# Kernel optimization log

Measured on AMD Instinct MI355X. Metric: run time of the kernel, lower is better.

Reference implementation:

```python
import jax, jax.numpy as jnp
import numpy as np

B, S, HID = 2, 2048, 2048
H, KV, D = 16, 4, 128
ROT = 64           # partial rotary dim (= cos.shape[-1])
EMB = 128          # router embedding dim
TAU, BASE = 0.4, 3.0
EPS = 1e-6


def rotate_half(x):
    h = x.shape[-1] // 2
    return jnp.concatenate([-x[..., h:], x[..., :h]], axis=-1)


def rmsnorm(x, w, eps=EPS):
    # Qwen3.5: zero-init weight, (1 + w) scaling, compute in fp32
    xf = x.astype(jnp.float32)
    o = xf * jax.lax.rsqrt(jnp.mean(xf * xf, axis=-1, keepdims=True) + eps)
    return (o * (1.0 + w.astype(jnp.float32))).astype(x.dtype)


def _rope_tables():
    inv_freq = 1.0 / (10000.0 ** (np.arange(0, ROT, 2, dtype=np.float32) / ROT))
    t = np.arange(S, dtype=np.float32)
    freqs = np.outer(t, inv_freq)                 # [S, ROT/2]
    emb = np.concatenate([freqs, freqs], axis=-1)  # [S, ROT]
    cos = np.broadcast_to(np.cos(emb), (B, S, ROT)).copy()
    sin = np.broadcast_to(np.sin(emb), (B, S, ROT)).copy()
    return jnp.asarray(cos), jnp.asarray(sin)


def setup_inputs() -> dict:
    key = jax.random.key(0)
    ks = jax.random.split(key, 10)
    sc = 0.02
    cos, sin = _rope_tables()
    return {
        "hidden_states": jax.random.normal(ks[0], (B, S, HID), jnp.float32),
        "cos": cos,
        "sin": sin,
        # projection weights stored as [in, out] (torch Linear weight transposed)
        "Wq": jax.random.normal(ks[1], (HID, H * D * 2), jnp.float32) * sc,
        "Wk": jax.random.normal(ks[2], (HID, KV * D), jnp.float32) * sc,
        "Wv": jax.random.normal(ks[3], (HID, KV * D), jnp.float32) * sc,
        "Wo": jax.random.normal(ks[4], (H * D, HID), jnp.float32) * sc,
        "q_norm_w": jnp.zeros((D,), jnp.float32),
        "k_norm_w": jnp.zeros((D,), jnp.float32),
        "Wr": jax.random.normal(ks[5], (HID, EMB), jnp.float32) * sc,   # router linear
        "Wd": jax.random.normal(ks[6], (EMB, D), jnp.float32) * sc,     # router decoder
        "ln_g": jnp.ones((EMB,), jnp.float32),
        "ln_b": jnp.zeros((EMB,), jnp.float32),
        "rnn_state": jnp.zeros((EMB,), jnp.float32),
    }


def _forward(hidden_states, cos, sin, Wq, Wk, Wv, Wo, q_norm_w, k_norm_w,
             Wr, Wd, ln_g, ln_b, rnn_state):
    b, s, _ = hidden_states.shape
    # doubled q_proj -> query + gate
    qkv = jnp.einsum('bsh,hd->bsd', hidden_states, Wq).reshape(b, s, H, 2 * D)
    q, gate = qkv[..., :D], qkv[..., D:]
    gate = gate.reshape(b, s, H * D)
    k = jnp.einsum('bsh,hd->bsd', hidden_states, Wk).reshape(b, s, KV, D)
    v = jnp.einsum('bsh,hd->bsd', hidden_states, Wv).reshape(b, s, KV, D)
    # per-head RMSNorm then [b, h, s, d]
    q = rmsnorm(q, q_norm_w).transpose(0, 2, 1, 3)
    k = rmsnorm(k, k_norm_w).transpose(0, 2, 1, 3)
    v = v.transpose(0, 2, 1, 3)

    # --- head-dim router (gumbel-sigmoid, straight-through hard round) ---
    emb = jnp.einsum('bsh,he->bse', hidden_states, Wr) + rnn_state
    mu = jnp.mean(emb, -1, keepdims=True)
    var = jnp.mean((emb - mu) ** 2, -1, keepdims=True)
    ln = (emb - mu) * jax.lax.rsqrt(var + 1e-5) * ln_g + ln_b
    logits = jnp.einsum('bse,ed->bsd', jax.nn.gelu(ln, approximate=False), Wd)
    gum = -jnp.log(jax.random.exponential(jax.random.key(42), logits.shape, jnp.float32))
    y_soft = jax.nn.sigmoid((logits + gum + BASE) / TAU)
    binary = jax.lax.stop_gradient(jnp.round(y_soft) - y_soft) + y_soft  # [b, s, D]
    mask = binary[:, None, :, :]  # broadcast over heads: [b, 1, s, D]

    q = q * mask
    k = k * mask

    # partial RoPE on first ROT dims (qk_index=None training path)
    c = cos[:, None, :, :]
    si = sin[:, None, :, :]
    def rope(x):
        xr, xp = x[..., :ROT], x[..., ROT:]
        return jnp.concatenate([xr * c + rotate_half(xr) * si, xp], axis=-1)
    q = rope(q)
    k = rope(k)

    # GQA: repeat kv heads
    rep = H // KV
    k = jnp.repeat(k, rep, axis=1)
    v = jnp.repeat(v, rep, axis=1)

    scores = jnp.einsum('bhqd,bhkd->bhqk', q, k) / np.sqrt(D).astype(np.float32)
    causal = jnp.tril(jnp.ones((s, s), bool))
    scores = jnp.where(causal, scores, jnp.finfo(jnp.float32).min)
    attn = jax.nn.softmax(scores.astype(jnp.float32), axis=-1).astype(q.dtype)
    out = jnp.einsum('bhqk,bhkd->bhqd', attn, v)
    out = out.transpose(0, 2, 1, 3).reshape(b, s, H * D)
    out = out * jax.nn.sigmoid(gate)   # output gate
    return jnp.einsum('bsd,dh->bsh', out, Wo)


def reference(hidden_states, cos, sin, Wq, Wk, Wv, Wo, q_norm_w, k_norm_w,
              Wr, Wd, ln_g, ln_b, rnn_state):
    return _forward(hidden_states, cos, sin, Wq, Wk, Wv, Wo, q_norm_w, k_norm_w,
                    Wr, Wd, ln_g, ln_b, rnn_state)
```

## Files before the change

kernel.cpp:

```cpp
#include <hip/hip_runtime.h>
#include <math.h>

typedef __bf16 bf16;
typedef bf16 bf16x8 __attribute__((ext_vector_type(8)));
typedef bf16 bf16x4 __attribute__((ext_vector_type(4)));
typedef float f32x4 __attribute__((ext_vector_type(4)));

#define BB 2
#define SS 2048
#define HIDN 2048
#define NH 16
#define NKV 4
#define DD 128
#define NROT 64
#define NPROJ 5248

__device__ __forceinline__ float waveAllReduceSum(float v) {
#pragma unroll
  for (int o = 1; o < 64; o <<= 1) v += __shfl_xor(v, o, 64);
  return v;
}

__device__ __forceinline__ int xcd_swz(int orig, int nwg) {
  return (orig & 7) * (nwg >> 3) + (orig >> 3);
}

__device__ __forceinline__ void gload16(const bf16* g, bf16* l) {
  __builtin_amdgcn_global_load_lds((const __attribute__((address_space(1))) void*)g,
                                   (__attribute__((address_space(3))) void*)l, 16, 0, 0);
}

__global__ __launch_bounds__(256) void cvt_bf16_k(const float* __restrict__ in,
                                                  bf16* __restrict__ out, int n) {
  int i = (blockIdx.x * 256 + threadIdx.x) * 4;
  if (i + 3 < n) {
    float4 v = *reinterpret_cast<const float4*>(in + i);
    bf16x4 o = {(bf16)v.x, (bf16)v.y, (bf16)v.z, (bf16)v.w};
    *reinterpret_cast<bf16x4*>(out + i) = o;
  }
}

__global__ __launch_bounds__(256) void transpose_cvt(const float* __restrict__ W,
                                                     bf16* __restrict__ WT, int K, int N,
                                                     int rowOff) {
  __shared__ bf16 tile[64][72];
  int n0 = blockIdx.x * 64, k0 = blockIdx.y * 64;
  int tx = threadIdx.x & 63, ty = threadIdx.x >> 6;
#pragma unroll
  for (int i = 0; i < 16; i++) {
    int k = ty + i * 4;
    tile[k][tx] = (bf16)W[(size_t)(k0 + k) * N + n0 + tx];
  }
  __syncthreads();
#pragma unroll
  for (int i = 0; i < 16; i++) {
    int n = ty + i * 4;
    WT[(size_t)(rowOff + n0 + n) * K + k0 + tx] = tile[tx][n];
  }
}

template <typename CT>
__global__ __launch_bounds__(256) void gemm_bt(const bf16* __restrict__ A,
                                               const bf16* __restrict__ Bt,
                                               CT* __restrict__ C, int M, int N, int K) {
  __shared__ bf16 lA[128 * 64];
  __shared__ bf16 lB[128 * 64];
  const int nbx = N >> 7;
  int wg = xcd_swz(blockIdx.x, gridDim.x);
  int bx = wg % nbx, by = wg / nbx;
  const int t = threadIdx.x;
  const int l = t & 63, w = t >> 6;
  const int wr = w >> 1, wc = w & 1;
  const int lr = l & 15, lhi = l >> 4;

  f32x4 acc[4][4];
#pragma unroll
  for (int m = 0; m < 4; m++)
#pragma unroll
    for (int n = 0; n < 4; n++) acc[m][n] = f32x4{0.f, 0.f, 0.f, 0.f};

  const int rowA0 = by * 128, rowB0 = bx * 128;
  const int nkt = K >> 6;
  for (int kt = 0; kt < nkt; ++kt) {
    __syncthreads();
#pragma unroll
    for (int it = 0; it < 4; ++it) {
      int slot = it * 256 + t;
      int row = slot >> 3, sl = slot & 7;
      gload16(A + (size_t)(rowA0 + row) * K + kt * 64 + ((sl ^ (row & 7)) << 3), lA + slot * 8);
      gload16(Bt + (size_t)(rowB0 + row) * K + kt * 64 + ((sl ^ (row & 7)) << 3), lB + slot * 8);
    }
    __syncthreads();
#pragma unroll
    for (int kc = 0; kc < 2; ++kc) {
      bf16x8 af[4], bg[4];
#pragma unroll
      for (int m = 0; m < 4; m++) {
        int row = wr * 64 + m * 16 + lr;
        af[m] = *reinterpret_cast<const bf16x8*>((char*)lA + row * 128 + (((kc * 4 + lhi) ^ (row & 7)) << 4));
      }
#pragma unroll
      for (int n = 0; n < 4; n++) {
        int row = wc * 64 + n * 16 + lr;
        bg[n] = *reinterpret_cast<const bf16x8*>((char*)lB + row * 128 + (((kc * 4 + lhi) ^ (row & 7)) << 4));
      }
      __builtin_amdgcn_s_setprio(1);
#pragma unroll
      for (int m = 0; m < 4; m++)
#pragma unroll
        for (int n = 0; n < 4; n++)
          acc[m][n] = __builtin_amdgcn_mfma_f32_16x16x32_bf16(af[m], bg[n], acc[m][n], 0, 0, 0);
      __builtin_amdgcn_s_setprio(0);
    }
  }
#pragma unroll
  for (int m = 0; m < 4; m++)
#pragma unroll
    for (int n = 0; n < 4; n++)
#pragma unroll
      for (int r = 0; r < 4; r++) {
        int grow = rowA0 + wr * 64 + m * 16 + lhi * 4 + r;
        int gcol = rowB0 + wc * 64 + n * 16 + lr;
        C[(size_t)grow * N + gcol] = (CT)acc[m][n][r];
      }
}

__device__ __forceinline__ unsigned rotl32(unsigned x, int r) { return (x << r) | (x >> (32 - r)); }

__device__ __forceinline__ float gumbel42(unsigned i) {
  const unsigned half = (unsigned)(BB * SS * DD) / 2u;
  unsigned x0, x1;
  int word;
  if (i < half) { x0 = i; x1 = i + half; word = 0; }
  else          { x0 = i - half; x1 = i; word = 1; }
  const unsigned k0 = 0u, k1 = 42u;
  const unsigned k2 = k0 ^ k1 ^ 0x1BD11BDAu;
  x0 += k0; x1 += k1;
#define TF_R(r) { x0 += x1; x1 = rotl32(x1, r); x1 ^= x0; }
  TF_R(13) TF_R(15) TF_R(26) TF_R(6)
  x0 += k1; x1 += k2 + 1u;
  TF_R(17) TF_R(29) TF_R(16) TF_R(24)
  x0 += k2; x1 += k0 + 2u;
  TF_R(13) TF_R(15) TF_R(26) TF_R(6)
  x0 += k0; x1 += k1 + 3u;
  TF_R(17) TF_R(29) TF_R(16) TF_R(24)
  x0 += k1; x1 += k2 + 4u;
  TF_R(13) TF_R(15) TF_R(26) TF_R(6)
  x0 += k2; x1 += k0 + 5u;
#undef TF_R
  unsigned bits = word ? x1 : x0;
  float u = __uint_as_float((bits >> 9) | 0x3f800000u) - 1.0f;
  float ex = -log1pf(-u);
  return -logf(ex);
}

__global__ __launch_bounds__(128) void mask_kernel(const bf16* __restrict__ qkva,
                                                   const float* __restrict__ rnn,
                                                   const float* __restrict__ lng,
                                                   const float* __restrict__ lnb,
                                                   const float* __restrict__ Wd,
                                                   bf16* __restrict__ maskb) {
  int row = blockIdx.x;
  int t = threadIdx.x;
  int l = t & 63, w = t >> 6;
  __shared__ float redm[2], redv[2], gsh[128];
  float e = (float)qkva[(size_t)row * NPROJ + 5120 + t] + rnn[t];
  float s1 = waveAllReduceSum(e);
  if (l == 0) redm[w] = s1;
  __syncthreads();
  float mu = (redm[0] + redm[1]) * (1.0f / 128.0f);
  float dv = (e - mu) * (e - mu);
  float s2 = waveAllReduceSum(dv);
  if (l == 0) redv[w] = s2;
  __syncthreads();
  float var = (redv[0] + redv[1]) * (1.0f / 128.0f);
  float ln = (e - mu) * rsqrtf(var + 1e-5f) * lng[t] + lnb[t];
  float g = 0.5f * ln * (1.0f + erff(ln * 0.7071067811865475f));
  gsh[t] = g;
  __syncthreads();
  float logit = 0.f;
#pragma unroll 8
  for (int e2 = 0; e2 < 128; e2++) logit += gsh[e2] * Wd[e2 * 128 + t];
  float gum = gumbel42((unsigned)(row * 128 + t));
  float x = (logit + gum + 3.0f) * 2.5f;
  float y = 1.0f / (1.0f + expf(-x));
  maskb[(size_t)row * 128 + t] = (bf16)rintf(y);
}

__global__ __launch_bounds__(256) void qgate_kernel(const bf16* __restrict__ qkva,
                                                    const bf16* __restrict__ maskb,
                                                    const float* __restrict__ qw,
                                                    const float* __restrict__ cosT,
                                                    const float* __restrict__ sinT,
                                                    bf16* __restrict__ wq,
                                                    bf16* __restrict__ sgate) {
  int t = threadIdx.x;
  int g = t >> 4, ln = t & 15;
  int hr = blockIdx.x * 16 + g;
  int h = hr & 15, row = hr >> 4;
  int b = row >> 11, s = row & 2047;
  const bf16* qp = qkva + (size_t)row * NPROJ + h * 256 + ln * 8;
  bf16x8 q8 = *reinterpret_cast<const bf16x8*>(qp);
  bf16x8 g8 = *reinterpret_cast<const bf16x8*>(qp + 128);
  bf16x8 m8 = *reinterpret_cast<const bf16x8*>(maskb + (size_t)row * 128 + ln * 8);
  float qf[8], ss = 0.f;
#pragma unroll
  for (int j = 0; j < 8; j++) { qf[j] = (float)q8[j]; ss += qf[j] * qf[j]; }
#pragma unroll
  for (int o = 1; o < 16; o <<= 1) ss += __shfl_xor(ss, o, 16);
  float rinv = rsqrtf(ss * (1.0f / 128.0f) + 1e-6f);
  alignas(16) float wv[8];
  const float4* qw4 = reinterpret_cast<const float4*>(qw);
  *reinterpret_cast<float4*>(&wv[0]) = qw4[ln * 2];
  *reinterpret_cast<float4*>(&wv[4]) = qw4[ln * 2 + 1];
  float qm[8];
#pragma unroll
  for (int j = 0; j < 8; j++) qm[j] = qf[j] * rinv * (1.0f + wv[j]) * (float)m8[j];
  alignas(16) float c8[8], s8[8];
  if (ln < 8) {
    const float4* c4 = reinterpret_cast<const float4*>(cosT + (size_t)row * 64);
    const float4* sn4 = reinterpret_cast<const float4*>(sinT + (size_t)row * 64);
    *reinterpret_cast<float4*>(&c8[0]) = c4[ln * 2];
    *reinterpret_cast<float4*>(&c8[4]) = c4[ln * 2 + 1];
    *reinterpret_cast<float4*>(&s8[0]) = sn4[ln * 2];
    *reinterpret_cast<float4*>(&s8[4]) = sn4[ln * 2 + 1];
  }
  float po[8];
#pragma unroll
  for (int j = 0; j < 8; j++) po[j] = __shfl_xor(qm[j], 4, 16);
  bf16x8 oq, og;
#pragma unroll
  for (int j = 0; j < 8; j++) {
    float ov;
    if (ln < 4) ov = qm[j] * c8[j] - po[j] * s8[j];
    else if (ln < 8) ov = qm[j] * c8[j] + po[j] * s8[j];
    else ov = qm[j];
    oq[j] = (bf16)(ov * 0.08838834764831845f);
    og[j] = (bf16)(1.0f / (1.0f + expf(-(float)g8[j])));
  }
  size_t o = ((size_t)((b * 16 + h) * 2048 + s)) * 128 + ln * 8;
  *reinterpret_cast<bf16x8*>(wq + o) = oq;
  *reinterpret_cast<bf16x8*>(sgate + o) = og;
}

__global__ __launch_bounds__(256) void k_kernel(const bf16* __restrict__ qkva,
                                                const bf16* __restrict__ maskb,
                                                const float* __restrict__ kw,
                                                const float* __restrict__ cosT,
                                                const float* __restrict__ sinT,
                                                bf16* __restrict__ wk) {
  int t = threadIdx.x;
  int g = t >> 4, ln = t & 15;
  int hr = blockIdx.x * 16 + g;
  int kv = hr & 3, row = hr >> 2;
  int b = row >> 11, s = row & 2047;
  const bf16* kp = qkva + (size_t)row * NPROJ + 4096 + kv * 128 + ln * 8;
  bf16x8 k8 = *reinterpret_cast<const bf16x8*>(kp);
  bf16x8 m8 = *reinterpret_cast<const bf16x8*>(maskb + (size_t)row * 128 + ln * 8);
  float kf[8], ss = 0.f;
#pragma unroll
  for (int j = 0; j < 8; j++) { kf[j] = (float)k8[j]; ss += kf[j] * kf[j]; }
#pragma unroll
  for (int o = 1; o < 16; o <<= 1) ss += __shfl_xor(ss, o, 16);
  float rinv = rsqrtf(ss * (1.0f / 128.0f) + 1e-6f);
  alignas(16) float wv[8];
  const float4* kw4 = reinterpret_cast<const float4*>(kw);
  *reinterpret_cast<float4*>(&wv[0]) = kw4[ln * 2];
  *reinterpret_cast<float4*>(&wv[4]) = kw4[ln * 2 + 1];
  float km[8];
#pragma unroll
  for (int j = 0; j < 8; j++) km[j] = kf[j] * rinv * (1.0f + wv[j]) * (float)m8[j];
  alignas(16) float c8[8], s8[8];
  if (ln < 8) {
    const float4* c4 = reinterpret_cast<const float4*>(cosT + (size_t)row * 64);
    const float4* sn4 = reinterpret_cast<const float4*>(sinT + (size_t)row * 64);
    *reinterpret_cast<float4*>(&c8[0]) = c4[ln * 2];
    *reinterpret_cast<float4*>(&c8[4]) = c4[ln * 2 + 1];
    *reinterpret_cast<float4*>(&s8[0]) = sn4[ln * 2];
    *reinterpret_cast<float4*>(&s8[4]) = sn4[ln * 2 + 1];
  }
  float po[8];
#pragma unroll
  for (int j = 0; j < 8; j++) po[j] = __shfl_xor(km[j], 4, 16);
  bf16x8 ok;
#pragma unroll
  for (int j = 0; j < 8; j++) {
    float ov;
    if (ln < 4) ov = km[j] * c8[j] - po[j] * s8[j];
    else if (ln < 8) ov = km[j] * c8[j] + po[j] * s8[j];
    else ov = km[j];
    ok[j] = (bf16)ov;
  }
  *reinterpret_cast<bf16x8*>(wk + ((size_t)((b * 4 + kv) * 2048 + s)) * 128 + ln * 8) = ok;
}

__global__ __launch_bounds__(256) void vt_kernel(const bf16* __restrict__ qkva,
                                                 bf16* __restrict__ wvt) {
  int dt = blockIdx.x & 1;
  int st = (blockIdx.x >> 1) & 31;
  int bkv = blockIdx.x >> 6;
  int b = bkv >> 2, kv = bkv & 3;
  __shared__ bf16 tl[64][72];
  int tx = threadIdx.x & 63, ty = threadIdx.x >> 6;
  int s0 = st * 64, d0 = dt * 64;
#pragma unroll
  for (int i = 0; i < 16; i++) {
    int srow = ty + i * 4;
    tl[srow][tx] = qkva[(size_t)(b * 2048 + s0 + srow) * NPROJ + 4608 + kv * 128 + d0 + tx];
  }
  __syncthreads();
#pragma unroll
  for (int i = 0; i < 16; i++) {
    int drow = ty + i * 4;
    wvt[(size_t)((b * 4 + kv) * 128 + d0 + drow) * 2048 + s0 + tx] = tl[tx][drow];
  }
}

__global__ __launch_bounds__(256) void attn_kernel(const bf16* __restrict__ wq,
                                                   const bf16* __restrict__ wk,
                                                   const bf16* __restrict__ wvt,
                                                   const bf16* __restrict__ sgate,
                                                   bf16* __restrict__ wattn) {
  __shared__ bf16 lK[64 * 128];
  __shared__ bf16 lV[128 * 64];
  __shared__ bf16 lP[4][16 * 64];
  int wg = xcd_swz(blockIdx.x, 512);
  int pair = wg & 15;
  int bh = wg >> 4;
  int b = bh >> 4, h = bh & 15, kvh = h >> 2;
  int t = threadIdx.x, l = t & 63, w = t >> 6;
  int lr = l & 15, lhi = l >> 4;

  const bf16* kbase = wk + (size_t)((b * 4 + kvh) * 2048) * 128;
  const bf16* vbase = wvt + (size_t)((b * 4 + kvh) * 128) * 2048;
  char* pb = (char*)(&lP[w][0]);

  for (int half = 0; half < 2; ++half) {
    int qb = half ? (31 - pair) : pair;
    const bf16* qbase = wq + (size_t)((b * 16 + h) * 2048 + qb * 64 + w * 16) * 128;
    bf16x8 aq[4];
#pragma unroll
    for (int kc = 0; kc < 4; kc++)
      aq[kc] = *reinterpret_cast<const bf16x8*>(qbase + (size_t)lr * 128 + kc * 32 + lhi * 8);

    f32x4 oacc[8];
#pragma unroll
    for (int db = 0; db < 8; db++) oacc[db] = f32x4{0.f, 0.f, 0.f, 0.f};
    float m_run = -3.0e38f, l_run = 0.f;
    int qrow_g = qb * 64 + w * 16 + lr;

    for (int tt = 0; tt <= qb; ++tt) {
      __syncthreads();
#pragma unroll
      for (int it = 0; it < 4; ++it) {
        int slot = it * 256 + t;
        int row = slot >> 4, sl = slot & 15;
        gload16(kbase + (size_t)(tt * 64 + row) * 128 + ((sl ^ (row & 7)) << 3), (bf16*)lK + slot * 8);
        int row2 = slot >> 3, sl2 = slot & 7;
        gload16(vbase + (size_t)row2 * 2048 + tt * 64 + ((sl2 ^ (row2 & 7)) << 3), (bf16*)lV + slot * 8);
      }
      __syncthreads();

      f32x4 sacc[4];
#pragma unroll
      for (int j = 0; j < 4; j++) sacc[j] = f32x4{0.f, 0.f, 0.f, 0.f};
      __builtin_amdgcn_s_setprio(1);
#pragma unroll
      for (int kc = 0; kc < 4; kc++)
#pragma unroll
        for (int j = 0; j < 4; j++) {
          int row = j * 16 + lr;
          bf16x8 ak = *reinterpret_cast<const bf16x8*>((char*)lK + row * 256 + (((kc * 4 + lhi) ^ (row & 7)) << 4));
          sacc[j] = __builtin_amdgcn_mfma_f32_16x16x32_bf16(ak, aq[kc], sacc[j], 0, 0, 0);
        }
      __builtin_amdgcn_s_setprio(0);

      if (tt == qb) {
#pragma unroll
        for (int j = 0; j < 4; j++)
#pragma unroll
          for (int r = 0; r < 4; r++) {
            int kg = tt * 64 + j * 16 + lhi * 4 + r;
            if (kg > qrow_g) sacc[j][r] = -1e30f;
          }
      }

      float m0 = fmaxf(fmaxf(sacc[0][0], sacc[0][1]), fmaxf(sacc[0][2], sacc[0][3]));
      float m1 = fmaxf(fmaxf(sacc[1][0], sacc[1][1]), fmaxf(sacc[1][2], sacc[1][3]));
      float m2 = fmaxf(fmaxf(sacc[2][0], sacc[2][1]), fmaxf(sacc[2][2], sacc[2][3]));
      float m3 = fmaxf(fmaxf(sacc[3][0], sacc[3][1]), fmaxf(sacc[3][2], sacc[3][3]));
      float mx = fmaxf(fmaxf(m0, m1), fmaxf(m2, m3));
      mx = fmaxf(mx, __shfl_xor(mx, 16, 64));
      mx = fmaxf(mx, __shfl_xor(mx, 32, 64));
      float mnew = fmaxf(m_run, mx);
      float p[4][4];
      float rs = 0.f;
#pragma unroll
      for (int j = 0; j < 4; j++) {
        float s0 = 0.f;
#pragma unroll
        for (int r = 0; r < 4; r++) {
          float pv = __expf(sacc[j][r] - mnew);
          p[j][r] = pv;
          s0 += pv;
        }
        rs += s0;
      }
      rs += __shfl_xor(rs, 16, 64);
      rs += __shfl_xor(rs, 32, 64);
      float corr = __expf(m_run - mnew);
      l_run = l_run * corr + rs;
      m_run = mnew;

      float corr_o[4];
#pragma unroll
      for (int r = 0; r < 4; r++) corr_o[r] = __shfl(corr, lhi * 4 + r, 64);
#pragma unroll
      for (int db = 0; db < 8; db++)
#pragma unroll
        for (int r = 0; r < 4; r++) oacc[db][r] *= corr_o[r];

#pragma unroll
      for (int j = 0; j < 4; j++) {
        bf16x4 p4 = {(bf16)p[j][0], (bf16)p[j][1], (bf16)p[j][2], (bf16)p[j][3]};
        *reinterpret_cast<bf16x4*>(pb + lr * 128 + ((j * 32 + lhi * 8) ^ ((lr & 7) << 4))) = p4;
      }
      bf16x8 pa[2];
#pragma unroll
      for (int kc2 = 0; kc2 < 2; kc2++)
        pa[kc2] = *reinterpret_cast<const bf16x8*>(pb + lr * 128 + ((kc2 * 64 + lhi * 16) ^ ((lr & 7) << 4)));
      __builtin_amdgcn_s_setprio(1);
#pragma unroll
      for (int kc2 = 0; kc2 < 2; kc2++)
#pragma unroll
        for (int db = 0; db < 8; db++) {
          int row = db * 16 + lr;
          bf16x8 bv = *reinterpret_cast<const bf16x8*>((char*)lV + row * 128 + (((kc2 * 4 + lhi) ^ (row & 7)) << 4));
          oacc[db] = __builtin_amdgcn_mfma_f32_16x16x32_bf16(pa[kc2], bv, oacc[db], 0, 0, 0);
        }
      __builtin_amdgcn_s_setprio(0);
    }

    float linv[4];
#pragma unroll
    for (int r = 0; r < 4; r++) linv[r] = 1.0f / __shfl(l_run, lhi * 4 + r, 64);
#pragma unroll
    for (int r = 0; r < 4; r++) {
      int srow = qb * 64 + w * 16 + lhi * 4 + r;
#pragma unroll
      for (int db = 0; db < 8; db++) {
        int dcol = db * 16 + lr;
        float g = (float)sgate[(size_t)((b * 16 + h) * 2048 + srow) * 128 + dcol];
        float ov = oacc[db][r] * linv[r] * g;
        wattn[(size_t)(b * 2048 + srow) * 2048 + h * 128 + dcol] = (bf16)ov;
      }
    }
  }
}

extern "C" void kernel_launch(void* const* d_in, const int* in_sizes, int n_in,
                              void* d_out, int out_size, void* d_ws, size_t ws_size,
                              hipStream_t stream) {
  const float* hidden = (const float*)d_in[0];
  const float* cosT = (const float*)d_in[1];
  const float* sinT = (const float*)d_in[2];
  const float* Wq = (const float*)d_in[3];
  const float* Wk = (const float*)d_in[4];
  const float* Wv = (const float*)d_in[5];
  const float* Wo = (const float*)d_in[6];
  const float* qw = (const float*)d_in[7];
  const float* kw = (const float*)d_in[8];
  const float* Wr = (const float*)d_in[9];
  const float* Wd = (const float*)d_in[10];
  const float* lng = (const float*)d_in[11];
  const float* lnb = (const float*)d_in[12];
  const float* rnn = (const float*)d_in[13];
  float* out = (float*)d_out;

  char* p = (char*)d_ws;
  auto alloc = [&](size_t bytes) { char* r = p; p += (bytes + 255) & ~(size_t)255; return r; };
  bf16* hb    = (bf16*)alloc((size_t)4096 * 2048 * 2);
  bf16* WTall = (bf16*)alloc((size_t)NPROJ * 2048 * 2);
  bf16* WoT   = (bf16*)alloc((size_t)2048 * 2048 * 2);
  bf16* qkva  = (bf16*)alloc((size_t)4096 * NPROJ * 2);
  bf16* maskb = (bf16*)alloc((size_t)4096 * 128 * 2);
  bf16* wqb   = (bf16*)alloc((size_t)2 * 16 * 2048 * 128 * 2);
  bf16* wkb   = (bf16*)alloc((size_t)2 * 4 * 2048 * 128 * 2);
  bf16* wvtb  = (bf16*)alloc((size_t)2 * 4 * 128 * 2048 * 2);
  bf16* sgb   = (bf16*)alloc((size_t)2 * 16 * 2048 * 128 * 2);
  bf16* wab   = (bf16*)alloc((size_t)4096 * 2048 * 2);
  if ((size_t)(p - (char*)d_ws) > ws_size) return;

  cvt_bf16_k<<<8192, 256, 0, stream>>>(hidden, hb, 4096 * 2048);
  transpose_cvt<<<dim3(64, 32), 256, 0, stream>>>(Wq, WTall, 2048, 4096, 0);
  transpose_cvt<<<dim3(8, 32), 256, 0, stream>>>(Wk, WTall, 2048, 512, 4096);
  transpose_cvt<<<dim3(8, 32), 256, 0, stream>>>(Wv, WTall, 2048, 512, 4608);
  transpose_cvt<<<dim3(2, 32), 256, 0, stream>>>(Wr, WTall, 2048, 128, 5120);
  transpose_cvt<<<dim3(32, 32), 256, 0, stream>>>(Wo, WoT, 2048, 2048, 0);

  gemm_bt<bf16><<<41 * 32, 256, 0, stream>>>(hb, WTall, qkva, 4096, NPROJ, 2048);

  mask_kernel<<<4096, 128, 0, stream>>>(qkva, rnn, lng, lnb, Wd, maskb);
  qgate_kernel<<<4096, 256, 0, stream>>>(qkva, maskb, qw, cosT, sinT, wqb, sgb);
  k_kernel<<<1024, 256, 0, stream>>>(qkva, maskb, kw, cosT, sinT, wkb);
  vt_kernel<<<512, 256, 0, stream>>>(qkva, wvtb);

  attn_kernel<<<512, 256, 0, stream>>>(wqb, wkb, wvtb, sgb, wab);

  gemm_bt<float><<<16 * 32, 256, 0, stream>>>(wab, WoT, out, 4096, 2048, 2048);
}
```

Baseline: 286.2 us.

## Double-buffer K/V tiles in attention, lazy softmax rescale, widen bf16 conversion

The attention kernel now double-buffers its K/V LDS tiles and prefetches the next tile while computing the current one. The two query blocks are merged into a single 33-iteration loop so the pipeline runs across the half boundary. Online softmax skips rescaling the output accumulators unless the running max grows by more than 8, which saves multiplies at the cost of a looser exponent bound. The fp32-to-bf16 conversion handles 8 elements per thread. Doubling LDS use may lower occupancy.

```diff
diff --git a/kernel.cpp b/kernel.cpp
--- a/kernel.cpp
+++ b/kernel.cpp
@@ -32,11 +32,13 @@
 
 __global__ __launch_bounds__(256) void cvt_bf16_k(const float* __restrict__ in,
                                                   bf16* __restrict__ out, int n) {
-  int i = (blockIdx.x * 256 + threadIdx.x) * 4;
-  if (i + 3 < n) {
-    float4 v = *reinterpret_cast<const float4*>(in + i);
-    bf16x4 o = {(bf16)v.x, (bf16)v.y, (bf16)v.z, (bf16)v.w};
-    *reinterpret_cast<bf16x4*>(out + i) = o;
+  int i = (blockIdx.x * 256 + threadIdx.x) * 8;
+  if (i + 7 < n) {
+    float4 v0 = *reinterpret_cast<const float4*>(in + i);
+    float4 v1 = *reinterpret_cast<const float4*>(in + i + 4);
+    bf16x8 o = {(bf16)v0.x, (bf16)v0.y, (bf16)v0.z, (bf16)v0.w,
+                (bf16)v1.x, (bf16)v1.y, (bf16)v1.z, (bf16)v1.w};
+    *reinterpret_cast<bf16x8*>(out + i) = o;
   }
 }
 
@@ -321,8 +323,8 @@
                                                    const bf16* __restrict__ wvt,
                                                    const bf16* __restrict__ sgate,
                                                    bf16* __restrict__ wattn) {
-  __shared__ bf16 lK[64 * 128];
-  __shared__ bf16 lV[128 * 64];
+  __shared__ bf16 lK[2][64 * 128];
+  __shared__ bf16 lV[2][128 * 64];
   __shared__ bf16 lP[4][16 * 64];
   int wg = xcd_swz(blockIdx.x, 512);
   int pair = wg & 15;
@@ -335,126 +337,160 @@
   const bf16* vbase = wvt + (size_t)((b * 4 + kvh) * 128) * 2048;
   char* pb = (char*)(&lP[w][0]);
 
-  for (int half = 0; half < 2; ++half) {
-    int qb = half ? (31 - pair) : pair;
-    const bf16* qbase = wq + (size_t)((b * 16 + h) * 2048 + qb * 64 + w * 16) * 128;
-    bf16x8 aq[4];
+  const int qb0 = pair, qb1 = 31 - pair;
+  const int n0 = qb0 + 1;
+
+  auto stage = [&](int buf, int tt) {
+#pragma unroll
+    for (int it = 0; it < 4; ++it) {
+      int slot = it * 256 + t;
+      int row = slot >> 4, sl = slot & 15;
+      gload16(kbase + (size_t)(tt * 64 + row) * 128 + ((sl ^ (row & 7)) << 3), lK[buf] + slot * 8);
+      int row2 = slot >> 3, sl2 = slot & 7;
+      gload16(vbase + (size_t)row2 * 2048 + tt * 64 + ((sl2 ^ (row2 & 7)) << 3), lV[buf] + slot * 8);
+    }
+  };
+
+  bf16x8 aq[4];
+  f32x4 oacc[8];
+  float m_run, l_run;
+  int half = 0, qb = qb0;
+
+  auto load_q = [&](int qbv) {
+    const bf16* qbase = wq + (size_t)((b * 16 + h) * 2048 + qbv * 64 + w * 16) * 128;
 #pragma unroll
     for (int kc = 0; kc < 4; kc++)
       aq[kc] = *reinterpret_cast<const bf16x8*>(qbase + (size_t)lr * 128 + kc * 32 + lhi * 8);
-
-    f32x4 oacc[8];
-#pragma unroll
-    for (int db = 0; db < 8; db++) oacc[db] = f32x4{0.f, 0.f, 0.f, 0.f};
-    float m_run = -3.0e38f, l_run = 0.f;
+  };
+  load_q(qb0);
+#pragma unroll
+  for (int db = 0; db < 8; db++) oacc[db] = f32x4{0.f, 0.f, 0.f, 0.f};
+  m_run = -3.0e38f;
+  l_run = 0.f;
+
+  stage(0, 0);
+  __syncthreads();
+  int cur = 0;
+
+  for (int i = 0; i < 33; ++i) {
+    int tt = (i < n0) ? i : i - n0;
+    if (i + 1 < 33) {
+      int tn = (i + 1 < n0) ? (i + 1) : (i + 1 - n0);
+      stage(cur ^ 1, tn);
+    }
     int qrow_g = qb * 64 + w * 16 + lr;
 
-    for (int tt = 0; tt <= qb; ++tt) {
-      __syncthreads();
-#pragma unroll
-      for (int it = 0; it < 4; ++it) {
-        int slot = it * 256 + t;
-        int row = slot >> 4, sl = slot & 15;
-        gload16(kbase + (size_t)(tt * 64 + row) * 128 + ((sl ^ (row & 7)) << 3), (bf16*)lK + slot * 8);
-        int row2 = slot >> 3, sl2 = slot & 7;
-        gload16(vbase + (size_t)row2 * 2048 + tt * 64 + ((sl2 ^ (row2 & 7)) << 3), (bf16*)lV + slot * 8);
-      }
-      __syncthreads();
-
-      f32x4 sacc[4];
-#pragma unroll
-      for (int j = 0; j < 4; j++) sacc[j] = f32x4{0.f, 0.f, 0.f, 0.f};
-      __builtin_amdgcn_s_setprio(1);
-#pragma unroll
-      for (int kc = 0; kc < 4; kc++)
-#pragma unroll
-        for (int j = 0; j < 4; j++) {
-          int row = j * 16 + lr;
-          bf16x8 ak = *reinterpret_cast<const bf16x8*>((char*)lK + row * 256 + (((kc * 4 + lhi) ^ (row & 7)) << 4));
-          sacc[j] = __builtin_amdgcn_mfma_f32_16x16x32_bf16(ak, aq[kc], sacc[j], 0, 0, 0);
+    f32x4 sacc[4];
+#pragma unroll
+    for (int j = 0; j < 4; j++) sacc[j] = f32x4{0.f, 0.f, 0.f, 0.f};
+    __builtin_amdgcn_s_setprio(1);
+#pragma unroll
+    for (int kc = 0; kc < 4; kc++)
+#pragma unroll
+      for (int j = 0; j < 4; j++) {
+        int row = j * 16 + lr;
+        bf16x8 ak = *reinterpret_cast<const bf16x8*>((char*)lK[cur] + row * 256 + (((kc * 4 + lhi) ^ (row & 7)) << 4));
+        sacc[j] = __builtin_amdgcn_mfma_f32_16x16x32_bf16(ak, aq[kc], sacc[j], 0, 0, 0);
+      }
+    __builtin_amdgcn_s_setprio(0);
+
+    if (tt == qb) {
+#pragma unroll
+      for (int j = 0; j < 4; j++)
+#pragma unroll
+        for (int r = 0; r < 4; r++) {
+          int kg = tt * 64 + j * 16 + lhi * 4 + r;
+          if (kg > qrow_g) sacc[j][r] = -1e30f;
         }
-      __builtin_amdgcn_s_setprio(0);
-
-      if (tt == qb) {
-#pragma unroll
-        for (int j = 0; j < 4; j++)
-#pragma unroll
-          for (int r = 0; r < 4; r++) {
-            int kg = tt * 64 + j * 16 + lhi * 4 + r;
-            if (kg > qrow_g) sacc[j][r] = -1e30f;
-          }
-      }
-
-      float m0 = fmaxf(fmaxf(sacc[0][0], sacc[0][1]), fmaxf(sacc[0][2], sacc[0][3]));
-      float m1 = fmaxf(fmaxf(sacc[1][0], sacc[1][1]), fmaxf(sacc[1][2], sacc[1][3]));
-      float m2 = fmaxf(fmaxf(sacc[2][0], sacc[2][1]), fmaxf(sacc[2][2], sacc[2][3]));
-      float m3 = fmaxf(fmaxf(sacc[3][0], sacc[3][1]), fmaxf(sacc[3][2], sacc[3][3]));
-      float mx = fmaxf(fmaxf(m0, m1), fmaxf(m2, m3));
-      mx = fmaxf(mx, __shfl_xor(mx, 16, 64));
-      mx = fmaxf(mx, __shfl_xor(mx, 32, 64));
+    }
+
+    float m0 = fmaxf(fmaxf(sacc[0][0], sacc[0][1]), fmaxf(sacc[0][2], sacc[0][3]));
+    float m1 = fmaxf(fmaxf(sacc[1][0], sacc[1][1]), fmaxf(sacc[1][2], sacc[1][3]));
+    float m2 = fmaxf(fmaxf(sacc[2][0], sacc[2][1]), fmaxf(sacc[2][2], sacc[2][3]));
+    float m3 = fmaxf(fmaxf(sacc[3][0], sacc[3][1]), fmaxf(sacc[3][2], sacc[3][3]));
+    float mx = fmaxf(fmaxf(m0, m1), fmaxf(m2, m3));
+    mx = fmaxf(mx, __shfl_xor(mx, 16, 64));
+    mx = fmaxf(mx, __shfl_xor(mx, 32, 64));
+
+    if (!__all(mx <= m_run + 8.0f)) {
       float mnew = fmaxf(m_run, mx);
-      float p[4][4];
-      float rs = 0.f;
-#pragma unroll
-      for (int j = 0; j < 4; j++) {
-        float s0 = 0.f;
-#pragma unroll
-        for (int r = 0; r < 4; r++) {
-          float pv = __expf(sacc[j][r] - mnew);
-          p[j][r] = pv;
-          s0 += pv;
+      float corr = __expf(m_run - mnew);
+      l_run *= corr;
+      m_run = mnew;
+      float corr_o[4];
+#pragma unroll
+      for (int r = 0; r < 4; r++) corr_o[r] = __shfl(corr, lhi * 4 + r, 64);
+#pragma unroll
+      for (int db = 0; db < 8; db++)
+#pragma unroll
+        for (int r = 0; r < 4; r++) oacc[db][r] *= corr_o[r];
+    }
+
+    float p[4][4];
+    float rs = 0.f;
+#pragma unroll
+    for (int j = 0; j < 4; j++) {
+      float s0 = 0.f;
+#pragma unroll
+      for (int r = 0; r < 4; r++) {
+        float pv = __expf(sacc[j][r] - m_run);
+        p[j][r] = pv;
+        s0 += pv;
+      }
+      rs += s0;
+    }
+    rs += __shfl_xor(rs, 16, 64);
+    rs += __shfl_xor(rs, 32, 64);
+    l_run += rs;
+
+#pragma unroll
+    for (int j = 0; j < 4; j++) {
+      bf16x4 p4 = {(bf16)p[j][0], (bf16)p[j][1], (bf16)p[j][2], (bf16)p[j][3]};
+      *reinterpret_cast<bf16x4*>(pb + lr * 128 + ((j * 32 + lhi * 8) ^ ((lr & 7) << 4))) = p4;
+    }
+    bf16x8 pa[2];
+#pragma unroll
+    for (int kc2 = 0; kc2 < 2; kc2++)
+      pa[kc2] = *reinterpret_cast<const bf16x8*>(pb + lr * 128 + ((kc2 * 64 + lhi * 16) ^ ((lr & 7) << 4)));
+    __builtin_amdgcn_s_setprio(1);
+#pragma unroll
+    for (int kc2 = 0; kc2 < 2; kc2++)
+#pragma unroll
+      for (int db = 0; db < 8; db++) {
+        int row = db * 16 + lr;
+        bf16x8 bv = *reinterpret_cast<const bf16x8*>((char*)lV[cur] + row * 128 + (((kc2 * 4 + lhi) ^ (row & 7)) << 4));
+        oacc[db] = __builtin_amdgcn_mfma_f32_16x16x32_bf16(pa[kc2], bv, oacc[db], 0, 0, 0);
+      }
+    __builtin_amdgcn_s_setprio(0);
+
+    if (tt == qb) {
+      float linv[4];
+#pragma unroll
+      for (int r = 0; r < 4; r++) linv[r] = 1.0f / __shfl(l_run, lhi * 4 + r, 64);
+#pragma unroll
+      for (int r = 0; r < 4; r++) {
+        int srow = qb * 64 + w * 16 + lhi * 4 + r;
+#pragma unroll
+        for (int db = 0; db < 8; db++) {
+          int dcol = db * 16 + lr;
+          float g = (float)sgate[(size_t)((b * 16 + h) * 2048 + srow) * 128 + dcol];
+          float ov = oacc[db][r] * linv[r] * g;
+          wattn[(size_t)(b * 2048 + srow) * 2048 + h * 128 + dcol] = (bf16)ov;
         }
-        rs += s0;
-      }
-      rs += __shfl_xor(rs, 16, 64);
-      rs += __shfl_xor(rs, 32, 64);
-      float corr = __expf(m_run - mnew);
-      l_run = l_run * corr + rs;
-      m_run = mnew;
-
-      float corr_o[4];
-#pragma unroll
-      for (int r = 0; r < 4; r++) corr_o[r] = __shfl(corr, lhi * 4 + r, 64);
-#pragma unroll
-      for (int db = 0; db < 8; db++)
-#pragma unroll
-        for (int r = 0; r < 4; r++) oacc[db][r] *= corr_o[r];
-
-#pragma unroll
-      for (int j = 0; j < 4; j++) {
-        bf16x4 p4 = {(bf16)p[j][0], (bf16)p[j][1], (bf16)p[j][2], (bf16)p[j][3]};
-        *reinterpret_cast<bf16x4*>(pb + lr * 128 + ((j * 32 + lhi * 8) ^ ((lr & 7) << 4))) = p4;
-      }
-      bf16x8 pa[2];
-#pragma unroll
-      for (int kc2 = 0; kc2 < 2; kc2++)
-        pa[kc2] = *reinterpret_cast<const bf16x8*>(pb + lr * 128 + ((kc2 * 64 + lhi * 16) ^ ((lr & 7) << 4)));
-      __builtin_amdgcn_s_setprio(1);
-#pragma unroll
-      for (int kc2 = 0; kc2 < 2; kc2++)
-#pragma unroll
-        for (int db = 0; db < 8; db++) {
-          int row = db * 16 + lr;
-          bf16x8 bv = *reinterpret_cast<const bf16x8*>((char*)lV + row * 128 + (((kc2 * 4 + lhi) ^ (row & 7)) << 4));
-          oacc[db] = __builtin_amdgcn_mfma_f32_16x16x32_bf16(pa[kc2], bv, oacc[db], 0, 0, 0);
-        }
-      __builtin_amdgcn_s_setprio(0);
-    }
-
-    float linv[4];
-#pragma unroll
-    for (int r = 0; r < 4; r++) linv[r] = 1.0f / __shfl(l_run, lhi * 4 + r, 64);
-#pragma unroll
-    for (int r = 0; r < 4; r++) {
-      int srow = qb * 64 + w * 16 + lhi * 4 + r;
-#pragma unroll
-      for (int db = 0; db < 8; db++) {
-        int dcol = db * 16 + lr;
-        float g = (float)sgate[(size_t)((b * 16 + h) * 2048 + srow) * 128 + dcol];
-        float ov = oacc[db][r] * linv[r] * g;
-        wattn[(size_t)(b * 2048 + srow) * 2048 + h * 128 + dcol] = (bf16)ov;
-      }
-    }
+      }
+      if (half == 0) {
+        half = 1;
+        qb = qb1;
+        load_q(qb1);
+#pragma unroll
+        for (int db = 0; db < 8; db++) oacc[db] = f32x4{0.f, 0.f, 0.f, 0.f};
+        m_run = -3.0e38f;
+        l_run = 0.f;
+      }
+    }
+
+    __syncthreads();
+    cur ^= 1;
   }
 }
 
@@ -491,7 +527,7 @@
   bf16* wab   = (bf16*)alloc((size_t)4096 * 2048 * 2);
   if ((size_t)(p - (char*)d_ws) > ws_size) return;
 
-  cvt_bf16_k<<<8192, 256, 0, stream>>>(hidden, hb, 4096 * 2048);
+  cvt_bf16_k<<<4096, 256, 0, stream>>>(hidden, hb, 4096 * 2048);
   transpose_cvt<<<dim3(64, 32), 256, 0, stream>>>(Wq, WTall, 2048, 4096, 0);
   transpose_cvt<<<dim3(8, 32), 256, 0, stream>>>(Wk, WTall, 2048, 512, 4096);
   transpose_cvt<<<dim3(8, 32), 256, 0, stream>>>(Wv, WTall, 2048, 512, 4608);
```

New measurement: 289.1 us. No clear change (+1.0%).
